# Kernel optimization log

Hardware: AMD Instinct MI355X
Metric: run time of the kernel (lower is better)

The kernel has to match this reference:

```python
import jax, jax.numpy as jnp
import numpy as np

DIM = 1024   # dim
T = 16       # maximum_time_steps
NT = 64      # num_templates
B = 2048     # batch
S = 77       # words per sentence


def setup_inputs() -> dict:
    key = jax.random.key(0)
    ks = jax.random.split(key, 16)
    p = lambda k, shp: jax.random.normal(k, shp, dtype=jnp.float32) * 0.02
    return {
        "text_feats": jax.random.normal(ks[0], (B, S, DIM), dtype=jnp.float32),
        "text_sentence_feats": jax.random.normal(ks[1], (B, DIM), dtype=jnp.float32),
        "textual_query": jax.random.normal(ks[2], (B, DIM), dtype=jnp.float32),
        "time_step": jax.random.randint(ks[3], (B,), 0, T),
        "W1_w": p(ks[4], (T, DIM, DIM)),   # T stacked [out,in] linears
        "W1_b": p(ks[5], (T, DIM)),
        "W2_w": p(ks[6], (DIM, 2 * DIM)),
        "W2_b": p(ks[7], (DIM,)),
        "m1_w": p(ks[8], (DIM, DIM)),
        "m1_b": p(ks[9], (DIM,)),
        "m2_w": p(ks[10], (DIM, DIM)),
        "m2_b": p(ks[11], (DIM,)),
        "m3_w": p(ks[12], (NT, DIM)),
        "m3_b": p(ks[13], (NT,)),
        "attn_w": p(ks[14], (1, DIM)),
        "attn_b": p(ks[15], (1,)),
    }


def reference(text_feats, text_sentence_feats, textual_query, time_step,
              W1_w, W1_b, W2_w, W2_b, m1_w, m1_b, m2_w, m2_b, m3_w, m3_b,
              attn_w, attn_b):
    # Time-indexed linear: T is small, so compute all T projections for every
    # sample and select per-sample (avoids materializing a [B,DIM,DIM] gather).
    all_proj = jnp.einsum('bc,toc->tbo', text_sentence_feats, W1_w) + W1_b[:, None, :]  # t b d
    x1 = jnp.take_along_axis(all_proj, time_step[None, :, None], axis=0)[0]  # b d
    # concat with textual query, project back to dim
    x = jnp.concatenate([x1, textual_query], axis=-1) @ W2_w.T + W2_b  # b d
    # 3-layer MLP -> template distribution
    h = jax.nn.relu(x @ m1_w.T + m1_b)
    h = jax.nn.relu(h @ m2_w.T + m2_b)
    template_distribution = jax.nn.softmax(h @ m3_w.T + m3_b, axis=-1)  # b #templates
    # soft attention over words: score each (x * word_feat) with a linear
    x_w = x[:, None, :] * text_feats  # b s c
    scores = jnp.einsum('bsc,c->bs', x_w, attn_w[0]) + attn_b[0]
    words_soft_distribution = jax.nn.softmax(scores, axis=-1)  # b s
    c_t = jnp.einsum('bs,bsc->bc', words_soft_distribution, text_feats)  # b c
    return template_distribution, words_soft_distribution, c_t
```

## Files before the change

kernel.cpp:

```cpp
#include <hip/hip_runtime.h>
#include <stdint.h>

typedef __bf16 bf16;
typedef bf16 bf16x8 __attribute__((ext_vector_type(8)));
typedef bf16 bf16x4 __attribute__((ext_vector_type(4)));
typedef float f32x4 __attribute__((ext_vector_type(4)));

#define DIM   1024
#define TMAX  16
#define NTPL  64
#define BATCH 2048
#define SLEN  77

__device__ __forceinline__ void gl_lds16(const void* g, void* l) {
  __builtin_amdgcn_global_load_lds(
      (const __attribute__((address_space(1))) void*)g,
      (__attribute__((address_space(3))) void*)l, 16, 0, 0);
}

__global__ void bucket_k(const int* __restrict__ ts, int* __restrict__ perm,
                         int* __restrict__ bstart) {
  __shared__ int cnt[TMAX], base[TMAX], cur[TMAX];
  int tid = threadIdx.x;
  if (tid < TMAX) { cnt[tid] = 0; cur[tid] = 0; }
  __syncthreads();
  for (int b = tid; b < BATCH; b += 256) atomicAdd(&cnt[ts[b]], 1);
  __syncthreads();
  if (tid == 0) {
    int a = 0;
    for (int t = 0; t < TMAX; ++t) { base[t] = a; bstart[t] = a; a += cnt[t]; }
    bstart[TMAX] = a;
  }
  __syncthreads();
  for (int b = tid; b < BATCH; b += 256) {
    int t = ts[b];
    perm[base[t] + atomicAdd(&cur[t], 1)] = b;
  }
}

__global__ void cvt_bf16_k(const float* __restrict__ src, bf16* __restrict__ dst) {
  int idx = blockIdx.x * 256 + threadIdx.x;
  float4 v = ((const float4*)src)[idx];
  bf16x4 o = {(bf16)v.x, (bf16)v.y, (bf16)v.z, (bf16)v.w};
  ((bf16x4*)dst)[idx] = o;
}

__global__ void cvt_tq_k(const float* __restrict__ tq, bf16* __restrict__ xcat) {
  int idx = blockIdx.x * 256 + threadIdx.x;
  int b = idx >> 8, c4 = idx & 255;
  float4 v = ((const float4*)(tq + (size_t)b * DIM))[c4];
  bf16x4 o = {(bf16)v.x, (bf16)v.y, (bf16)v.z, (bf16)v.w};
  *(bf16x4*)(xcat + (size_t)b * 2 * DIM + DIM + c4 * 4) = o;
}

__global__ __launch_bounds__(256, 2) void gemm_bt(
    const bf16* __restrict__ A, int lda, const bf16* __restrict__ B, int ldb,
    const float* __restrict__ bias, bf16* __restrict__ C, int ldc,
    float* __restrict__ Cf, int N, int K, int relu) {
  __shared__ bf16 As[128 * 32];
  __shared__ bf16 Bs[128 * 32];
  const int tid = threadIdx.x;
  const int rowBase = blockIdx.y * 128, colBase = blockIdx.x * 128;

  const bf16* ag[2]; const bf16* bg[2];
  bf16* al[2]; bf16* bl[2];
#pragma unroll
  for (int i = 0; i < 2; ++i) {
    int j = tid + i * 256;
    int r = j >> 2, kq = j & 3;
    ag[i] = A + (size_t)(rowBase + r) * lda + kq * 8;
    int bn = colBase + r; if (bn > N - 1) bn = N - 1;
    bg[i] = B + (size_t)bn * ldb + kq * 8;
    al[i] = As + j * 8;
    bl[i] = Bs + j * 8;
  }
  const int wave = tid >> 6, lane = tid & 63;
  const int wm = wave >> 1, wn = wave & 1;
  const int mr = lane & 15, quad = lane >> 4;

  f32x4 acc[4][4];
#pragma unroll
  for (int i = 0; i < 4; ++i)
#pragma unroll
    for (int j = 0; j < 4; ++j) acc[i][j] = (f32x4){0.f, 0.f, 0.f, 0.f};

  for (int k0 = 0; k0 < K; k0 += 32) {
    __syncthreads();
#pragma unroll
    for (int i = 0; i < 2; ++i) {
      gl_lds16(ag[i] + k0, al[i]);
      gl_lds16(bg[i] + k0, bl[i]);
    }
    __syncthreads();
    bf16x8 af[4], bfr[4];
#pragma unroll
    for (int i = 0; i < 4; ++i)
      af[i] = *(const bf16x8*)&As[(wm * 64 + i * 16 + mr) * 32 + quad * 8];
#pragma unroll
    for (int j = 0; j < 4; ++j)
      bfr[j] = *(const bf16x8*)&Bs[(wn * 64 + j * 16 + mr) * 32 + quad * 8];
#pragma unroll
    for (int i = 0; i < 4; ++i)
#pragma unroll
      for (int j = 0; j < 4; ++j)
        acc[i][j] = __builtin_amdgcn_mfma_f32_16x16x32_bf16(af[i], bfr[j], acc[i][j], 0, 0, 0);
  }

  const int r0 = quad * 4;
#pragma unroll
  for (int i = 0; i < 4; ++i) {
    int gm = rowBase + wm * 64 + i * 16 + r0;
#pragma unroll
    for (int j = 0; j < 4; ++j) {
      int gn = colBase + wn * 64 + j * 16 + mr;
      if (gn < N) {
        float bv = bias ? bias[gn] : 0.f;
#pragma unroll
        for (int r = 0; r < 4; ++r) {
          float v = acc[i][j][r] + bv;
          if (relu) v = fmaxf(v, 0.f);
          C[(size_t)(gm + r) * ldc + gn] = (bf16)v;
          if (Cf) Cf[(size_t)(gm + r) * ldc + gn] = v;
        }
      }
    }
  }
}

__global__ __launch_bounds__(256, 2) void gemm_stage1(
    const bf16* __restrict__ tsbf, const bf16* __restrict__ W1bf,
    const float* __restrict__ W1b, const int* __restrict__ perm,
    const int* __restrict__ bstart, bf16* __restrict__ xcat) {
  const int t = blockIdx.z;
  const int s0 = bstart[t];
  const int cnt = bstart[t + 1] - s0;
  const int by = blockIdx.y;
  if (by * 128 >= cnt) return;
  __shared__ bf16 As[128 * 32];
  __shared__ bf16 Bs[128 * 32];
  const int tid = threadIdx.x;
  const int colBase = blockIdx.x * 128;
  const bf16* Bmat = W1bf + ((size_t)t << 20);

  const bf16* ag[2]; const bf16* bg[2];
  bf16* al[2]; bf16* bl[2];
#pragma unroll
  for (int i = 0; i < 2; ++i) {
    int j = tid + i * 256;
    int r = j >> 2, kq = j & 3;
    int lr = by * 128 + r;
    int src = perm[s0 + (lr < cnt ? lr : 0)];
    ag[i] = tsbf + (size_t)src * DIM + kq * 8;
    bg[i] = Bmat + (size_t)(colBase + r) * DIM + kq * 8;
    al[i] = As + j * 8;
    bl[i] = Bs + j * 8;
  }
  const int wave = tid >> 6, lane = tid & 63;
  const int wm = wave >> 1, wn = wave & 1;
  const int mr = lane & 15, quad = lane >> 4;

  f32x4 acc[4][4];
#pragma unroll
  for (int i = 0; i < 4; ++i)
#pragma unroll
    for (int j = 0; j < 4; ++j) acc[i][j] = (f32x4){0.f, 0.f, 0.f, 0.f};

  for (int k0 = 0; k0 < DIM; k0 += 32) {
    __syncthreads();
#pragma unroll
    for (int i = 0; i < 2; ++i) {
      gl_lds16(ag[i] + k0, al[i]);
      gl_lds16(bg[i] + k0, bl[i]);
    }
    __syncthreads();
    bf16x8 af[4], bfr[4];
#pragma unroll
    for (int i = 0; i < 4; ++i)
      af[i] = *(const bf16x8*)&As[(wm * 64 + i * 16 + mr) * 32 + quad * 8];
#pragma unroll
    for (int j = 0; j < 4; ++j)
      bfr[j] = *(const bf16x8*)&Bs[(wn * 64 + j * 16 + mr) * 32 + quad * 8];
#pragma unroll
    for (int i = 0; i < 4; ++i)
#pragma unroll
      for (int j = 0; j < 4; ++j)
        acc[i][j] = __builtin_amdgcn_mfma_f32_16x16x32_bf16(af[i], bfr[j], acc[i][j], 0, 0, 0);
  }

  const int r0 = quad * 4;
#pragma unroll
  for (int i = 0; i < 4; ++i) {
    int lr = by * 128 + wm * 64 + i * 16 + r0;
#pragma unroll
    for (int j = 0; j < 4; ++j) {
      int gn = colBase + wn * 64 + j * 16 + mr;
      float bv = W1b[t * DIM + gn];
#pragma unroll
      for (int r = 0; r < 4; ++r) {
        if (lr + r < cnt) {
          int bidx = perm[s0 + lr + r];
          xcat[(size_t)bidx * 2 * DIM + gn] = (bf16)(acc[i][j][r] + bv);
        }
      }
    }
  }
}

__global__ __launch_bounds__(256) void softmax64_k(const bf16* __restrict__ logits,
                                                   float* __restrict__ out) {
  int row = blockIdx.x * 4 + (threadIdx.x >> 6);
  int lane = threadIdx.x & 63;
  float v = (float)logits[row * NTPL + lane];
  float mx = v;
#pragma unroll
  for (int o = 32; o; o >>= 1) mx = fmaxf(mx, __shfl_xor(mx, o));
  float e = __expf(v - mx);
  float s = e;
#pragma unroll
  for (int o = 32; o; o >>= 1) s += __shfl_xor(s, o);
  out[row * NTPL + lane] = e / s;
}

__global__ __launch_bounds__(256) void attn_k(
    const float* __restrict__ x, const float* __restrict__ attn_w,
    const float* __restrict__ attn_b, const float* __restrict__ feats,
    float* __restrict__ words, float* __restrict__ ct) {
  const int b = blockIdx.x;
  const int tid = threadIdx.x;
  const float* fb = feats + (size_t)b * SLEN * DIM;
  float4 aw = ((const float4*)attn_w)[tid];
  float4 xv = ((const float4*)(x + (size_t)b * DIM))[tid];
  const float v0 = xv.x * aw.x, v1 = xv.y * aw.y, v2 = xv.z * aw.z, v3 = xv.w * aw.w;
  const float ab = attn_b[0];
  __shared__ float red[4];
  __shared__ float sc[SLEN];
  const int wave = tid >> 6, lane = tid & 63;
  float m = -1e30f, l = 0.f;
  float a0 = 0.f, a1 = 0.f, a2 = 0.f, a3 = 0.f;
  float4 f = ((const float4*)fb)[tid];
  for (int s = 0; s < SLEN; ++s) {
    float4 fn = make_float4(0.f, 0.f, 0.f, 0.f);
    if (s + 1 < SLEN) fn = ((const float4*)(fb + (size_t)(s + 1) * DIM))[tid];
    float p = f.x * v0 + f.y * v1 + f.z * v2 + f.w * v3;
#pragma unroll
    for (int o = 32; o; o >>= 1) p += __shfl_down(p, o);
    if (lane == 0) red[wave] = p;
    __syncthreads();
    float score = red[0] + red[1] + red[2] + red[3] + ab;
    __syncthreads();
    if (tid == 0) sc[s] = score;
    float mn = fmaxf(m, score);
    float scale = __expf(m - mn);
    float w = __expf(score - mn);
    l = l * scale + w;
    a0 = a0 * scale + w * f.x;
    a1 = a1 * scale + w * f.y;
    a2 = a2 * scale + w * f.z;
    a3 = a3 * scale + w * f.w;
    m = mn;
    f = fn;
  }
  __syncthreads();
  float inv = 1.f / l;
  if (tid < SLEN) words[(size_t)b * SLEN + tid] = __expf(sc[tid] - m) * inv;
  float4 o; o.x = a0 * inv; o.y = a1 * inv; o.z = a2 * inv; o.w = a3 * inv;
  ((float4*)(ct + (size_t)b * DIM))[tid] = o;
}

extern "C" void kernel_launch(void* const* d_in, const int* in_sizes, int n_in,
                              void* d_out, int out_size, void* d_ws, size_t ws_size,
                              hipStream_t stream) {
  const float* feats = (const float*)d_in[0];
  const float* tsent = (const float*)d_in[1];
  const float* tq    = (const float*)d_in[2];
  const int*   tstep = (const int*)d_in[3];
  const float* W1w = (const float*)d_in[4];
  const float* W1b = (const float*)d_in[5];
  const float* W2w = (const float*)d_in[6];
  const float* W2b = (const float*)d_in[7];
  const float* m1w = (const float*)d_in[8];
  const float* m1b = (const float*)d_in[9];
  const float* m2w = (const float*)d_in[10];
  const float* m2b = (const float*)d_in[11];
  const float* m3w = (const float*)d_in[12];
  const float* m3b = (const float*)d_in[13];
  const float* attw = (const float*)d_in[14];
  const float* attb = (const float*)d_in[15];

  char* p = (char*)d_ws;
  auto alloc = [&](size_t bytes) { char* q = p; p += (bytes + 255) & ~(size_t)255; return q; };
  int*  perm   = (int*)alloc(BATCH * 4);
  int*  bstart = (int*)alloc(17 * 4);
  bf16* tsbf = (bf16*)alloc((size_t)BATCH * DIM * 2);
  bf16* W1bf = (bf16*)alloc((size_t)TMAX * DIM * DIM * 2);
  bf16* W2bf = (bf16*)alloc((size_t)DIM * 2 * DIM * 2);
  bf16* m1bf = (bf16*)alloc((size_t)DIM * DIM * 2);
  bf16* m2bf = (bf16*)alloc((size_t)DIM * DIM * 2);
  bf16* m3bf = (bf16*)alloc((size_t)NTPL * DIM * 2);
  bf16* xcat = (bf16*)alloc((size_t)BATCH * 2 * DIM * 2);
  bf16* xbf  = (bf16*)alloc((size_t)BATCH * DIM * 2);
  float* xf  = (float*)alloc((size_t)BATCH * DIM * 4);
  bf16* h1   = (bf16*)alloc((size_t)BATCH * DIM * 2);
  bf16* h2   = (bf16*)alloc((size_t)BATCH * DIM * 2);
  bf16* lg   = (bf16*)alloc((size_t)BATCH * NTPL * 2);

  float* out_td = (float*)d_out;
  float* out_w  = out_td + (size_t)BATCH * NTPL;
  float* out_ct = out_w + (size_t)BATCH * SLEN;

  bucket_k<<<1, 256, 0, stream>>>(tstep, perm, bstart);
  cvt_bf16_k<<<(TMAX * DIM * DIM) / 1024, 256, 0, stream>>>(W1w, W1bf);
  cvt_bf16_k<<<(BATCH * DIM) / 1024, 256, 0, stream>>>(tsent, tsbf);
  cvt_bf16_k<<<(DIM * 2 * DIM) / 1024, 256, 0, stream>>>(W2w, W2bf);
  cvt_bf16_k<<<(DIM * DIM) / 1024, 256, 0, stream>>>(m1w, m1bf);
  cvt_bf16_k<<<(DIM * DIM) / 1024, 256, 0, stream>>>(m2w, m2bf);
  cvt_bf16_k<<<(NTPL * DIM) / 1024, 256, 0, stream>>>(m3w, m3bf);
  cvt_tq_k<<<(BATCH * DIM) / 1024, 256, 0, stream>>>(tq, xcat);

  gemm_stage1<<<dim3(DIM / 128, BATCH / 128, TMAX), 256, 0, stream>>>(
      tsbf, W1bf, W1b, perm, bstart, xcat);
  gemm_bt<<<dim3(DIM / 128, BATCH / 128), 256, 0, stream>>>(
      xcat, 2 * DIM, W2bf, 2 * DIM, W2b, xbf, DIM, xf, DIM, 2 * DIM, 0);
  gemm_bt<<<dim3(DIM / 128, BATCH / 128), 256, 0, stream>>>(
      xbf, DIM, m1bf, DIM, m1b, h1, DIM, nullptr, DIM, DIM, 1);
  gemm_bt<<<dim3(DIM / 128, BATCH / 128), 256, 0, stream>>>(
      h1, DIM, m2bf, DIM, m2b, h2, DIM, nullptr, DIM, DIM, 1);
  gemm_bt<<<dim3(1, BATCH / 128), 256, 0, stream>>>(
      h2, DIM, m3bf, DIM, m3b, lg, NTPL, nullptr, NTPL, DIM, 0);
  softmax64_k<<<BATCH / 4, 256, 0, stream>>>(lg, out_td);
  attn_k<<<BATCH, 256, 0, stream>>>(xf, attw, attb, feats, out_w, out_ct);
}
```

Before: 1.076 ms.

## Shrink GEMM tiles to 64x64 with double-buffered LDS; parallelize attention over waves

The GEMM kernels move from 128x128 tiles to 64x64 tiles with double-buffered LDS loads, which gives more blocks (the m3 GEMM and stage1 buckets in particular) and overlaps the next tile's global-to-LDS load with compute. The attention kernel now has each wave process every fourth word over the full DIM, with its own online softmax. The per-wave states are merged through shared memory at the end, which removes the two block-wide barriers per word. The cost is lower data reuse per tile in the GEMMs and 16KB of extra LDS in the attention kernel.

```diff
diff --git a/kernel.cpp b/kernel.cpp
--- a/kernel.cpp
+++ b/kernel.cpp
@@ -53,81 +53,78 @@
   *(bf16x4*)(xcat + (size_t)b * 2 * DIM + DIM + c4 * 4) = o;
 }
 
-__global__ __launch_bounds__(256, 2) void gemm_bt(
+__global__ __launch_bounds__(256, 4) void gemm_bt64(
     const bf16* __restrict__ A, int lda, const bf16* __restrict__ B, int ldb,
     const float* __restrict__ bias, bf16* __restrict__ C, int ldc,
     float* __restrict__ Cf, int N, int K, int relu) {
-  __shared__ bf16 As[128 * 32];
-  __shared__ bf16 Bs[128 * 32];
+  __shared__ bf16 As[2][64 * 32];
+  __shared__ bf16 Bs[2][64 * 32];
   const int tid = threadIdx.x;
-  const int rowBase = blockIdx.y * 128, colBase = blockIdx.x * 128;
-
-  const bf16* ag[2]; const bf16* bg[2];
-  bf16* al[2]; bf16* bl[2];
-#pragma unroll
-  for (int i = 0; i < 2; ++i) {
-    int j = tid + i * 256;
-    int r = j >> 2, kq = j & 3;
-    ag[i] = A + (size_t)(rowBase + r) * lda + kq * 8;
-    int bn = colBase + r; if (bn > N - 1) bn = N - 1;
-    bg[i] = B + (size_t)bn * ldb + kq * 8;
-    al[i] = As + j * 8;
-    bl[i] = Bs + j * 8;
-  }
+  const int rowBase = blockIdx.y * 64, colBase = blockIdx.x * 64;
+
+  const int r = tid >> 2, kq = tid & 3;
+  const bf16* ag = A + (size_t)(rowBase + r) * lda + kq * 8;
+  int bn = colBase + r; if (bn > N - 1) bn = N - 1;
+  const bf16* bg = B + (size_t)bn * ldb + kq * 8;
+
   const int wave = tid >> 6, lane = tid & 63;
   const int wm = wave >> 1, wn = wave & 1;
   const int mr = lane & 15, quad = lane >> 4;
 
-  f32x4 acc[4][4];
-#pragma unroll
-  for (int i = 0; i < 4; ++i)
-#pragma unroll
-    for (int j = 0; j < 4; ++j) acc[i][j] = (f32x4){0.f, 0.f, 0.f, 0.f};
-
-  for (int k0 = 0; k0 < K; k0 += 32) {
+  f32x4 acc[2][2];
+#pragma unroll
+  for (int i = 0; i < 2; ++i)
+#pragma unroll
+    for (int j = 0; j < 2; ++j) acc[i][j] = (f32x4){0.f, 0.f, 0.f, 0.f};
+
+  gl_lds16(ag, &As[0][tid * 8]);
+  gl_lds16(bg, &Bs[0][tid * 8]);
+  __syncthreads();
+
+  const int nk = K >> 5;
+  for (int t = 0; t < nk; ++t) {
+    const int cur = t & 1;
+    if (t + 1 < nk) {
+      gl_lds16(ag + (t + 1) * 32, &As[cur ^ 1][tid * 8]);
+      gl_lds16(bg + (t + 1) * 32, &Bs[cur ^ 1][tid * 8]);
+    }
+    bf16x8 af[2], bfr[2];
+#pragma unroll
+    for (int i = 0; i < 2; ++i)
+      af[i] = *(const bf16x8*)&As[cur][(wm * 32 + i * 16 + mr) * 32 + quad * 8];
+#pragma unroll
+    for (int j = 0; j < 2; ++j)
+      bfr[j] = *(const bf16x8*)&Bs[cur][(wn * 32 + j * 16 + mr) * 32 + quad * 8];
+#pragma unroll
+    for (int i = 0; i < 2; ++i)
+#pragma unroll
+      for (int j = 0; j < 2; ++j)
+        acc[i][j] = __builtin_amdgcn_mfma_f32_16x16x32_bf16(af[i], bfr[j], acc[i][j], 0, 0, 0);
     __syncthreads();
-#pragma unroll
-    for (int i = 0; i < 2; ++i) {
-      gl_lds16(ag[i] + k0, al[i]);
-      gl_lds16(bg[i] + k0, bl[i]);
-    }
-    __syncthreads();
-    bf16x8 af[4], bfr[4];
-#pragma unroll
-    for (int i = 0; i < 4; ++i)
-      af[i] = *(const bf16x8*)&As[(wm * 64 + i * 16 + mr) * 32 + quad * 8];
-#pragma unroll
-    for (int j = 0; j < 4; ++j)
-      bfr[j] = *(const bf16x8*)&Bs[(wn * 64 + j * 16 + mr) * 32 + quad * 8];
-#pragma unroll
-    for (int i = 0; i < 4; ++i)
-#pragma unroll
-      for (int j = 0; j < 4; ++j)
-        acc[i][j] = __builtin_amdgcn_mfma_f32_16x16x32_bf16(af[i], bfr[j], acc[i][j], 0, 0, 0);
   }
 
   const int r0 = quad * 4;
 #pragma unroll
-  for (int i = 0; i < 4; ++i) {
-    int gm = rowBase + wm * 64 + i * 16 + r0;
-#pragma unroll
-    for (int j = 0; j < 4; ++j) {
-      int gn = colBase + wn * 64 + j * 16 + mr;
+  for (int i = 0; i < 2; ++i) {
+    int gm = rowBase + wm * 32 + i * 16 + r0;
+#pragma unroll
+    for (int j = 0; j < 2; ++j) {
+      int gn = colBase + wn * 32 + j * 16 + mr;
       if (gn < N) {
         float bv = bias ? bias[gn] : 0.f;
 #pragma unroll
-        for (int r = 0; r < 4; ++r) {
-          float v = acc[i][j][r] + bv;
+        for (int rr = 0; rr < 4; ++rr) {
+          float v = acc[i][j][rr] + bv;
           if (relu) v = fmaxf(v, 0.f);
-          C[(size_t)(gm + r) * ldc + gn] = (bf16)v;
-          if (Cf) Cf[(size_t)(gm + r) * ldc + gn] = v;
+          C[(size_t)(gm + rr) * ldc + gn] = (bf16)v;
+          if (Cf) Cf[(size_t)(gm + rr) * ldc + gn] = v;
         }
       }
     }
   }
 }
 
-__global__ __launch_bounds__(256, 2) void gemm_stage1(
+__global__ __launch_bounds__(256, 4) void gemm_stage1(
     const bf16* __restrict__ tsbf, const bf16* __restrict__ W1bf,
     const float* __restrict__ W1b, const int* __restrict__ perm,
     const int* __restrict__ bstart, bf16* __restrict__ xcat) {
@@ -135,71 +132,68 @@
   const int s0 = bstart[t];
   const int cnt = bstart[t + 1] - s0;
   const int by = blockIdx.y;
-  if (by * 128 >= cnt) return;
-  __shared__ bf16 As[128 * 32];
-  __shared__ bf16 Bs[128 * 32];
+  if (by * 64 >= cnt) return;
+  __shared__ bf16 As[2][64 * 32];
+  __shared__ bf16 Bs[2][64 * 32];
   const int tid = threadIdx.x;
-  const int colBase = blockIdx.x * 128;
+  const int colBase = blockIdx.x * 64;
   const bf16* Bmat = W1bf + ((size_t)t << 20);
 
-  const bf16* ag[2]; const bf16* bg[2];
-  bf16* al[2]; bf16* bl[2];
-#pragma unroll
-  for (int i = 0; i < 2; ++i) {
-    int j = tid + i * 256;
-    int r = j >> 2, kq = j & 3;
-    int lr = by * 128 + r;
-    int src = perm[s0 + (lr < cnt ? lr : 0)];
-    ag[i] = tsbf + (size_t)src * DIM + kq * 8;
-    bg[i] = Bmat + (size_t)(colBase + r) * DIM + kq * 8;
-    al[i] = As + j * 8;
-    bl[i] = Bs + j * 8;
-  }
+  const int r = tid >> 2, kq = tid & 3;
+  const int lr0 = by * 64 + r;
+  const int src = perm[s0 + (lr0 < cnt ? lr0 : 0)];
+  const bf16* ag = tsbf + (size_t)src * DIM + kq * 8;
+  const bf16* bg = Bmat + (size_t)(colBase + r) * DIM + kq * 8;
+
   const int wave = tid >> 6, lane = tid & 63;
   const int wm = wave >> 1, wn = wave & 1;
   const int mr = lane & 15, quad = lane >> 4;
 
-  f32x4 acc[4][4];
-#pragma unroll
-  for (int i = 0; i < 4; ++i)
-#pragma unroll
-    for (int j = 0; j < 4; ++j) acc[i][j] = (f32x4){0.f, 0.f, 0.f, 0.f};
-
-  for (int k0 = 0; k0 < DIM; k0 += 32) {
+  f32x4 acc[2][2];
+#pragma unroll
+  for (int i = 0; i < 2; ++i)
+#pragma unroll
+    for (int j = 0; j < 2; ++j) acc[i][j] = (f32x4){0.f, 0.f, 0.f, 0.f};
+
+  gl_lds16(ag, &As[0][tid * 8]);
+  gl_lds16(bg, &Bs[0][tid * 8]);
+  __syncthreads();
+
+  const int nk = DIM >> 5;
+  for (int t2 = 0; t2 < nk; ++t2) {
+    const int cur = t2 & 1;
+    if (t2 + 1 < nk) {
+      gl_lds16(ag + (t2 + 1) * 32, &As[cur ^ 1][tid * 8]);
+      gl_lds16(bg + (t2 + 1) * 32, &Bs[cur ^ 1][tid * 8]);
+    }
+    bf16x8 af[2], bfr[2];
+#pragma unroll
+    for (int i = 0; i < 2; ++i)
+      af[i] = *(const bf16x8*)&As[cur][(wm * 32 + i * 16 + mr) * 32 + quad * 8];
+#pragma unroll
+    for (int j = 0; j < 2; ++j)
+      bfr[j] = *(const bf16x8*)&Bs[cur][(wn * 32 + j * 16 + mr) * 32 + quad * 8];
+#pragma unroll
+    for (int i = 0; i < 2; ++i)
+#pragma unroll
+      for (int j = 0; j < 2; ++j)
+        acc[i][j] = __builtin_amdgcn_mfma_f32_16x16x32_bf16(af[i], bfr[j], acc[i][j], 0, 0, 0);
     __syncthreads();
-#pragma unroll
-    for (int i = 0; i < 2; ++i) {
-      gl_lds16(ag[i] + k0, al[i]);
-      gl_lds16(bg[i] + k0, bl[i]);
-    }
-    __syncthreads();
-    bf16x8 af[4], bfr[4];
-#pragma unroll
-    for (int i = 0; i < 4; ++i)
-      af[i] = *(const bf16x8*)&As[(wm * 64 + i * 16 + mr) * 32 + quad * 8];
-#pragma unroll
-    for (int j = 0; j < 4; ++j)
-      bfr[j] = *(const bf16x8*)&Bs[(wn * 64 + j * 16 + mr) * 32 + quad * 8];
-#pragma unroll
-    for (int i = 0; i < 4; ++i)
-#pragma unroll
-      for (int j = 0; j < 4; ++j)
-        acc[i][j] = __builtin_amdgcn_mfma_f32_16x16x32_bf16(af[i], bfr[j], acc[i][j], 0, 0, 0);
   }
 
   const int r0 = quad * 4;
 #pragma unroll
-  for (int i = 0; i < 4; ++i) {
-    int lr = by * 128 + wm * 64 + i * 16 + r0;
-#pragma unroll
-    for (int j = 0; j < 4; ++j) {
-      int gn = colBase + wn * 64 + j * 16 + mr;
+  for (int i = 0; i < 2; ++i) {
+    int lr = by * 64 + wm * 32 + i * 16 + r0;
+#pragma unroll
+    for (int j = 0; j < 2; ++j) {
+      int gn = colBase + wn * 32 + j * 16 + mr;
       float bv = W1b[t * DIM + gn];
 #pragma unroll
-      for (int r = 0; r < 4; ++r) {
-        if (lr + r < cnt) {
-          int bidx = perm[s0 + lr + r];
-          xcat[(size_t)bidx * 2 * DIM + gn] = (bf16)(acc[i][j][r] + bv);
+      for (int rr = 0; rr < 4; ++rr) {
+        if (lr + rr < cnt) {
+          int bidx = perm[s0 + lr + rr];
+          xcat[(size_t)bidx * 2 * DIM + gn] = (bf16)(acc[i][j][rr] + bv);
         }
       }
     }
@@ -227,44 +221,92 @@
     float* __restrict__ words, float* __restrict__ ct) {
   const int b = blockIdx.x;
   const int tid = threadIdx.x;
+  const int wave = tid >> 6, lane = tid & 63;
   const float* fb = feats + (size_t)b * SLEN * DIM;
-  float4 aw = ((const float4*)attn_w)[tid];
-  float4 xv = ((const float4*)(x + (size_t)b * DIM))[tid];
-  const float v0 = xv.x * aw.x, v1 = xv.y * aw.y, v2 = xv.z * aw.z, v3 = xv.w * aw.w;
+
+  float4 vj[4];
+#pragma unroll
+  for (int j = 0; j < 4; ++j) {
+    int d = 4 * lane + 256 * j;
+    float4 xv = *(const float4*)(x + (size_t)b * DIM + d);
+    float4 aw = *(const float4*)(attn_w + d);
+    vj[j] = make_float4(xv.x * aw.x, xv.y * aw.y, xv.z * aw.z, xv.w * aw.w);
+  }
   const float ab = attn_b[0];
-  __shared__ float red[4];
-  __shared__ float sc[SLEN];
-  const int wave = tid >> 6, lane = tid & 63;
+
+  __shared__ float s_acc[4][DIM];
+  __shared__ float s_m[4], s_l[4], s_sc[SLEN];
+
   float m = -1e30f, l = 0.f;
-  float a0 = 0.f, a1 = 0.f, a2 = 0.f, a3 = 0.f;
-  float4 f = ((const float4*)fb)[tid];
-  for (int s = 0; s < SLEN; ++s) {
-    float4 fn = make_float4(0.f, 0.f, 0.f, 0.f);
-    if (s + 1 < SLEN) fn = ((const float4*)(fb + (size_t)(s + 1) * DIM))[tid];
-    float p = f.x * v0 + f.y * v1 + f.z * v2 + f.w * v3;
-#pragma unroll
-    for (int o = 32; o; o >>= 1) p += __shfl_down(p, o);
-    if (lane == 0) red[wave] = p;
-    __syncthreads();
-    float score = red[0] + red[1] + red[2] + red[3] + ab;
-    __syncthreads();
-    if (tid == 0) sc[s] = score;
+  float4 acc[4];
+#pragma unroll
+  for (int j = 0; j < 4; ++j) acc[j] = make_float4(0.f, 0.f, 0.f, 0.f);
+
+  float4 f[4];
+  {
+    const float* fr = fb + (size_t)wave * DIM;
+#pragma unroll
+    for (int j = 0; j < 4; ++j) f[j] = *(const float4*)(fr + 4 * lane + 256 * j);
+  }
+
+  for (int s = wave; s < SLEN; s += 4) {
+    float4 fn[4];
+    if (s + 4 < SLEN) {
+      const float* fr = fb + (size_t)(s + 4) * DIM;
+#pragma unroll
+      for (int j = 0; j < 4; ++j) fn[j] = *(const float4*)(fr + 4 * lane + 256 * j);
+    }
+    float p = 0.f;
+#pragma unroll
+    for (int j = 0; j < 4; ++j)
+      p += f[j].x * vj[j].x + f[j].y * vj[j].y + f[j].z * vj[j].z + f[j].w * vj[j].w;
+#pragma unroll
+    for (int o = 32; o; o >>= 1) p += __shfl_xor(p, o);
+    float score = p + ab;
+    if (lane == 0) s_sc[s] = score;
+
     float mn = fmaxf(m, score);
     float scale = __expf(m - mn);
     float w = __expf(score - mn);
     l = l * scale + w;
-    a0 = a0 * scale + w * f.x;
-    a1 = a1 * scale + w * f.y;
-    a2 = a2 * scale + w * f.z;
-    a3 = a3 * scale + w * f.w;
+#pragma unroll
+    for (int j = 0; j < 4; ++j) {
+      acc[j].x = acc[j].x * scale + w * f[j].x;
+      acc[j].y = acc[j].y * scale + w * f[j].y;
+      acc[j].z = acc[j].z * scale + w * f[j].z;
+      acc[j].w = acc[j].w * scale + w * f[j].w;
+    }
     m = mn;
-    f = fn;
-  }
-  __syncthreads();
-  float inv = 1.f / l;
-  if (tid < SLEN) words[(size_t)b * SLEN + tid] = __expf(sc[tid] - m) * inv;
-  float4 o; o.x = a0 * inv; o.y = a1 * inv; o.z = a2 * inv; o.w = a3 * inv;
+    if (s + 4 < SLEN) {
+#pragma unroll
+      for (int j = 0; j < 4; ++j) f[j] = fn[j];
+    }
+  }
+
+#pragma unroll
+  for (int j = 0; j < 4; ++j)
+    *(float4*)&s_acc[wave][4 * lane + 256 * j] = acc[j];
+  if (lane == 0) { s_m[wave] = m; s_l[wave] = l; }
+  __syncthreads();
+
+  const float gm = fmaxf(fmaxf(s_m[0], s_m[1]), fmaxf(s_m[2], s_m[3]));
+  float sc0 = __expf(s_m[0] - gm), sc1 = __expf(s_m[1] - gm);
+  float sc2 = __expf(s_m[2] - gm), sc3 = __expf(s_m[3] - gm);
+  const float L = s_l[0] * sc0 + s_l[1] * sc1 + s_l[2] * sc2 + s_l[3] * sc3;
+  const float inv = 1.f / L;
+
+  float4 a0 = *(const float4*)&s_acc[0][4 * tid];
+  float4 a1 = *(const float4*)&s_acc[1][4 * tid];
+  float4 a2 = *(const float4*)&s_acc[2][4 * tid];
+  float4 a3 = *(const float4*)&s_acc[3][4 * tid];
+  float4 o;
+  o.x = (a0.x * sc0 + a1.x * sc1 + a2.x * sc2 + a3.x * sc3) * inv;
+  o.y = (a0.y * sc0 + a1.y * sc1 + a2.y * sc2 + a3.y * sc3) * inv;
+  o.z = (a0.z * sc0 + a1.z * sc1 + a2.z * sc2 + a3.z * sc3) * inv;
+  o.w = (a0.w * sc0 + a1.w * sc1 + a2.w * sc2 + a3.w * sc3) * inv;
   ((float4*)(ct + (size_t)b * DIM))[tid] = o;
+
+  if (tid < SLEN) words[(size_t)b * SLEN + tid] = __expf(s_sc[tid] - gm) * inv;
 }
 
 extern "C" void kernel_launch(void* const* d_in, const int* in_sizes, int n_in,
@@ -317,15 +359,15 @@
   cvt_bf16_k<<<(NTPL * DIM) / 1024, 256, 0, stream>>>(m3w, m3bf);
   cvt_tq_k<<<(BATCH * DIM) / 1024, 256, 0, stream>>>(tq, xcat);
 
-  gemm_stage1<<<dim3(DIM / 128, BATCH / 128, TMAX), 256, 0, stream>>>(
+  gemm_stage1<<<dim3(DIM / 64, BATCH / 64, TMAX), 256, 0, stream>>>(
       tsbf, W1bf, W1b, perm, bstart, xcat);
-  gemm_bt<<<dim3(DIM / 128, BATCH / 128), 256, 0, stream>>>(
+  gemm_bt64<<<dim3(DIM / 64, BATCH / 64), 256, 0, stream>>>(
       xcat, 2 * DIM, W2bf, 2 * DIM, W2b, xbf, DIM, xf, DIM, 2 * DIM, 0);
-  gemm_bt<<<dim3(DIM / 128, BATCH / 128), 256, 0, stream>>>(
+  gemm_bt64<<<dim3(DIM / 64, BATCH / 64), 256, 0, stream>>>(
       xbf, DIM, m1bf, DIM, m1b, h1, DIM, nullptr, DIM, DIM, 1);
-  gemm_bt<<<dim3(DIM / 128, BATCH / 128), 256, 0, stream>>>(
+  gemm_bt64<<<dim3(DIM / 64, BATCH / 64), 256, 0, stream>>>(
       h1, DIM, m2bf, DIM, m2b, h2, DIM, nullptr, DIM, DIM, 1);
-  gemm_bt<<<dim3(1, BATCH / 128), 256, 0, stream>>>(
+  gemm_bt64<<<dim3(1, BATCH / 64), 256, 0, stream>>>(
       h2, DIM, m3bf, DIM, m3b, lg, NTPL, nullptr, NTPL, DIM, 0);
   softmax64_k<<<BATCH / 4, 256, 0, stream>>>(lg, out_td);
   attn_k<<<BATCH, 256, 0, stream>>>(xf, attw, attb, feats, out_w, out_ct);
```

Result: faster. 1.022 ms (-5.0%).
